# Kernel optimization log

Measured on AMD Instinct MI355X. Metric: run time of the kernel, lower is better.

Reference implementation:

```python
import jax, jax.numpy as jnp
import numpy as np

# module hyperparams (match init_kwargs)
C, K, S, RATIO, GC = 64, 7, 2, 2, 16
G = C // GC                      # 4 groups
KK = K * K                       # 49
NS = int(RATIO * S)              # 4
NN = NS * NS                     # 16
PAD = (K - 1) // 2               # 3
C1_IN = G * (2 * K * GC + KK)    # 1092
C1_OUT = G * NN * KK // 10       # 313
C2_OUT = G * NN * KK             # 3136
EPS = 1e-5


def _unfold(x, k, s, p):
    # torch.nn.Unfold: patches ordered (C, ki, kj) channel-major
    B, Cc, H, W = x.shape
    xp = jnp.pad(x, ((0, 0), (0, 0), (p, p), (p, p)))
    Ho = (H + 2 * p - k) // s + 1
    Wo = (W + 2 * p - k) // s + 1
    rows = jnp.arange(Ho)[:, None] * s + jnp.arange(k)[None, :]      # (Ho,k)
    cols = jnp.arange(Wo)[:, None] * s + jnp.arange(k)[None, :]      # (Wo,k)
    pat = xp[:, :, rows[:, :, None, None], cols[None, None, :, :]]   # (B,C,Ho,k,Wo,k)
    return pat.transpose(0, 1, 3, 5, 2, 4)                            # (B,C,k,k,Ho,Wo)


def setup_inputs() -> dict:
    key = jax.random.key(0)
    ks = jax.random.split(key, 5)
    x = jax.random.normal(ks[0], (8, C, 64, 64), dtype=jnp.float32)
    w1 = jax.random.normal(ks[1], (C1_OUT, C1_IN), dtype=jnp.float32) * 0.02
    gamma = jnp.ones((C1_OUT,), dtype=jnp.float32)   # BN weight (constant_init 1)
    beta = jnp.zeros((C1_OUT,), dtype=jnp.float32)   # BN bias
    w2 = jax.random.normal(ks[2], (C2_OUT, C1_OUT), dtype=jnp.float32) * 0.02
    b2 = jnp.zeros((C2_OUT,), dtype=jnp.float32)
    return {"x": x, "w1": w1, "gamma": gamma, "beta": beta, "w2": w2, "b2": b2}


def reference(x, w1, gamma, beta, w2, b2):
    B, _, H, W = x.shape
    pat = _unfold(x, K, S, PAD)                          # (B,C,K,K,Ho,Wo)
    Ho, Wo = pat.shape[-2], pat.shape[-1]
    xg = pat.reshape(B, G, GC, K, K, Ho, Wo)
    # three axis-wise max pools -> per-pixel descriptor
    x1 = xg.max(axis=2).reshape(B, G * K * K, Ho, Wo)
    x2 = xg.max(axis=3).reshape(B, G * GC * K, Ho, Wo)
    x3 = xg.max(axis=4).reshape(B, G * GC * K, Ho, Wo)
    feat = jnp.concatenate([x1, x2, x3], axis=1)         # (B, C1_IN, Ho, Wo)
    # conv1: 1x1 conv (no bias) + BN (batch stats) + ReLU
    h = jnp.einsum('bchw,oc->bohw', feat, w1)
    mu = h.mean(axis=(0, 2, 3), keepdims=True)
    var = h.var(axis=(0, 2, 3), keepdims=True)
    h = gamma[None, :, None, None] * (h - mu) * jax.lax.rsqrt(var + EPS) + beta[None, :, None, None]
    h = jax.nn.relu(h)
    # conv2: 1x1 conv with bias
    h2 = jnp.einsum('bchw,oc->bohw', h, w2) + b2[None, :, None, None]
    wt = h2.reshape(B, G, KK, NN, Ho, Wo)
    wt = jax.nn.softmax(wt, axis=2)                      # softmax over kernel positions
    # softmax-weighted patch reduction (mean over k*k)
    xk = xg.reshape(B, G, GC, KK, Ho, Wo)
    out = jnp.einsum('bgckhw,bgknhw->bgcnhw', xk, wt) / KK
    out = out.reshape(B, C, NS, NS, Ho, Wo)
    out = out.transpose(0, 1, 4, 2, 5, 3).reshape(B, C, Ho * NS, Wo * NS)
    return out
```

## Files before the change

### kernel.cpp

```cpp
#include <hip/hip_runtime.h>

namespace {
constexpr int kB    = 8;
constexpr int kC    = 64;
constexpr int kH    = 64, kW = 64;
constexpr int kNP   = 8192;
constexpr int kC1In = 1092;
constexpr int kKP   = 1152;
constexpr int kC1Out= 313;
constexpr int kC2Out= 3136;
constexpr int kC1P  = 320;
constexpr int kRowS = 56;
constexpr int kPosS = 16 * kRowS + 8;
constexpr int kPreFeat = 2048;
constexpr int kPreW2   = 490;
constexpr int kPreW1   = 1440;
constexpr int kPreBlocks = kPreFeat + kPreW2 + kPreW1;
}

typedef __attribute__((ext_vector_type(8))) short bf16x8;
typedef __attribute__((ext_vector_type(8))) _Float16 f16x8;
typedef __attribute__((ext_vector_type(2))) _Float16 h16x2;
typedef __attribute__((ext_vector_type(4))) float f32x4;

__device__ __forceinline__ unsigned short f2bf(float f) {
    unsigned u = __float_as_uint(f);
    unsigned r = (u + 0x7fffu + ((u >> 16) & 1u)) >> 16;
    return (unsigned short)r;
}
__device__ __forceinline__ float bf2f(unsigned short h) {
    return __uint_as_float(((unsigned)h) << 16);
}

__global__ __launch_bounds__(256) void k_pre(const float* __restrict__ x,
        const float* __restrict__ w1, const float* __restrict__ w2,
        unsigned short* __restrict__ feat_bf, unsigned short* __restrict__ w1s,
        bf16x8* __restrict__ w2t, float* __restrict__ stats) {
    __shared__ float xs[16 * 7 * 40];
    int tid = threadIdx.x;
    int bid = blockIdx.x;

    if (bid < kPreFeat) {
        int g = bid >> 9, pt = bid & 511;
        int p0 = pt * 16;
        int b = p0 >> 10, i = (p0 >> 5) & 31, j0 = p0 & 31;
        int y0 = 2 * i - 3, xbase = 2 * j0 - 3;
        const float* xb = x + ((size_t)(b * 64 + g * 16) << 12);

        for (int idx = tid; idx < 16 * 7 * 40; idx += 256) {
            int ch = idx / 280, r2 = idx - ch * 280;
            int row = r2 / 40, col = r2 - row * 40;
            int yy = y0 + row, xx = xbase + col;
            float v = 0.f;
            if ((unsigned)yy < 64u && (unsigned)xx < 64u)
                v = xb[(ch << 12) + (yy << 6) + xx];
            xs[idx] = v;
        }
        __syncthreads();

        for (int pos = 0; pos < 16; ++pos) {
            for (int c = tid; c < 273; c += 256) {
                float m = -INFINITY;
                int cg;
                if (c < 49) {
                    int a = c / 7, bk = c - a * 7;
                    int base = a * 40 + 2 * pos + bk;
                    #pragma unroll
                    for (int ch = 0; ch < 16; ++ch) m = fmaxf(m, xs[ch * 280 + base]);
                    cg = g * 49 + c;
                } else if (c < 161) {
                    int r = c - 49;
                    int ch = r / 7, bk = r - ch * 7;
                    int base = ch * 280 + 2 * pos + bk;
                    #pragma unroll
                    for (int a = 0; a < 7; ++a) m = fmaxf(m, xs[base + a * 40]);
                    cg = 196 + g * 112 + r;
                } else {
                    int r = c - 161;
                    int ch = r / 7, a = r - ch * 7;
                    int base = ch * 280 + a * 40 + 2 * pos;
                    #pragma unroll
                    for (int bk = 0; bk < 7; ++bk) m = fmaxf(m, xs[base + bk]);
                    cg = 644 + g * 112 + r;
                }
                feat_bf[(size_t)(p0 + pos) * kKP + cg] = f2bf(m);
            }
        }
        if (g == 3) {
            for (int idx = tid; idx < 16 * 60; idx += 256) {
                int pos = idx / 60, c = idx - pos * 60;
                feat_bf[(size_t)(p0 + pos) * kKP + 1092 + c] = 0;
            }
        }
    } else if (bid < kPreFeat + kPreW2) {
        int idx = (bid - kPreFeat) * 256 + tid;
        int lane = idx & 63;
        int t = (idx >> 6) % 10;
        int k = (idx / 640) % 49;
        int g = idx / 31360;
        int n = lane & 15, c0 = t * 32 + ((lane >> 4) << 3);
        int row = g * 784 + k * 16 + n;
        bf16x8 hi;
        #pragma unroll
        for (int e = 0; e < 8; ++e) {
            int c = c0 + e;
            float v = (c < kC1Out) ? w2[(size_t)row * kC1Out + c] : 0.f;
            hi[e] = (short)f2bf(v);
        }
        w2t[idx] = hi;
    } else {
        int idx = (bid - kPreFeat - kPreW2) * 256 + tid;
        if (idx < 640) stats[idx] = 0.f;
        int r = idx / kKP, c = idx - r * kKP;
        float v = (r < kC1Out && c < kC1In) ? w1[(size_t)r * kC1In + c] : 0.f;
        w1s[idx] = f2bf(v);
    }
}

__global__ __launch_bounds__(512) void k_gemm1(
        const unsigned short* __restrict__ feat_bf, const unsigned short* __restrict__ w1s,
        unsigned short* __restrict__ hb16, float* __restrict__ sum_, float* __restrict__ sumsq_) {
    __shared__ unsigned short Ald[128 * 64];
    __shared__ unsigned short Bld[64 * 64];
    __shared__ float lsum[64], lsq[64];
    int tid = threadIdx.x;
    int lane = tid & 63, wv = tid >> 6;
    int row0 = blockIdx.x * 128, col0 = blockIdx.y * 64;
    int wr = wv >> 1, wc = wv & 1;
    int srow = lane >> 3;
    int soct = (lane & 7) ^ srow;
    int frow = lane & 15, fk = lane >> 4;

    f32x4 acc[2][2] = {};
    for (int k0 = 0; k0 < kKP; k0 += 64) {
        #pragma unroll
        for (int qq = 0; qq < 3; ++qq) {
            int q = wv + qq * 8;
            const unsigned short* srcbase;
            unsigned short* dst;
            int grow;
            if (q < 16) { grow = row0 + q * 8 + srow; srcbase = feat_bf; dst = Ald + q * 512; }
            else        { grow = col0 + (q - 16) * 8 + srow; srcbase = w1s; dst = Bld + (q - 16) * 512; }
            const unsigned short* src = srcbase + (size_t)grow * kKP + k0 + soct * 8;
            __builtin_amdgcn_global_load_lds(
                (const __attribute__((address_space(1))) unsigned int*)src,
                (__attribute__((address_space(3))) unsigned int*)dst, 16, 0, 0);
        }
        __syncthreads();
        #pragma unroll
        for (int ks = 0; ks < 2; ++ks) {
            int oct = ks * 4 + fk;
            bf16x8 a0, a1, b0, b1;
            { int r = wr * 32 + frow;      a0 = *(const bf16x8*)(Ald + (r * 8 + (oct ^ (r & 7))) * 8); }
            { int r = wr * 32 + 16 + frow; a1 = *(const bf16x8*)(Ald + (r * 8 + (oct ^ (r & 7))) * 8); }
            { int r = wc * 32 + frow;      b0 = *(const bf16x8*)(Bld + (r * 8 + (oct ^ (r & 7))) * 8); }
            { int r = wc * 32 + 16 + frow; b1 = *(const bf16x8*)(Bld + (r * 8 + (oct ^ (r & 7))) * 8); }
            acc[0][0] = __builtin_amdgcn_mfma_f32_16x16x32_bf16(a0, b0, acc[0][0], 0, 0, 0);
            acc[0][1] = __builtin_amdgcn_mfma_f32_16x16x32_bf16(a0, b1, acc[0][1], 0, 0, 0);
            acc[1][0] = __builtin_amdgcn_mfma_f32_16x16x32_bf16(a1, b0, acc[1][0], 0, 0, 0);
            acc[1][1] = __builtin_amdgcn_mfma_f32_16x16x32_bf16(a1, b1, acc[1][1], 0, 0, 0);
        }
        __syncthreads();
    }

    if (tid < 64) { lsum[tid] = 0.f; lsq[tid] = 0.f; }
    __syncthreads();
    #pragma unroll
    for (int j = 0; j < 2; ++j) {
        int col_l = wc * 32 + j * 16 + (lane & 15);
        float s = 0.f, sq = 0.f;
        #pragma unroll
        for (int i = 0; i < 2; ++i) {
            int mrow = row0 + wr * 32 + i * 16 + (lane >> 4) * 4;
            #pragma unroll
            for (int r = 0; r < 4; ++r) {
                float v = acc[i][j][r];
                hb16[(size_t)(mrow + r) * kC1P + col0 + col_l] = f2bf(v);
                s += v; sq += v * v;
            }
        }
        s  += __shfl_xor(s, 16);  s  += __shfl_xor(s, 32);
        sq += __shfl_xor(sq, 16); sq += __shfl_xor(sq, 32);
        if (lane < 16) {
            atomicAdd(&lsum[col_l], s);
            atomicAdd(&lsq[col_l], sq);
        }
    }
    __syncthreads();
    if (tid < 64 && col0 + tid < kC1Out) {
        atomicAdd(&sum_[col0 + tid], lsum[tid]);
        atomicAdd(&sumsq_[col0 + tid], lsq[tid]);
    }
}

__global__ void k_split_h(const unsigned short* __restrict__ hb16,
                          const float* __restrict__ sum_, const float* __restrict__ sumsq_,
                          const float* __restrict__ gamma, const float* __restrict__ beta,
                          bf16x8* __restrict__ ht_hi) {
    int idx = blockIdx.x * 256 + threadIdx.x;
    int lane = idx & 63;
    int t = (idx >> 6) % 10;
    int ptile = idx / 640;
    int pos = ptile * 16 + (lane & 15);
    int c0 = t * 32 + ((lane >> 4) << 3);
    bf16x8 raw = *(const bf16x8*)(hb16 + (size_t)pos * kC1P + c0);
    bf16x8 hi;
    #pragma unroll
    for (int e = 0; e < 8; ++e) {
        int c = c0 + e;
        float v = 0.f;
        if (c < kC1Out) {
            float mu  = sum_[c]   * (1.f / kNP);
            float var = sumsq_[c] * (1.f / kNP) - mu * mu;
            float sc  = gamma[c] * rsqrtf(var + 1e-5f);
            float sh  = beta[c] - mu * sc;
            v = fmaxf(bf2f((unsigned short)raw[e]) * sc + sh, 0.f);
        }
        hi[e] = (short)f2bf(v);
    }
    ht_hi[idx] = hi;
}

__global__ __launch_bounds__(512) void k_fused(
        const bf16x8* __restrict__ ht_hi, const bf16x8* __restrict__ w2t,
        const float* __restrict__ b2, const float* __restrict__ x,
        float* __restrict__ out) {
    __shared__ _Float16 wtb[32 * kPosS];
    __shared__ float invt[512];
    __shared__ bf16x8 htl[1280];
    int tid = threadIdx.x;
    int lane = tid & 63, wv = tid >> 6;
    int bid = blockIdx.x;
    int g = bid >> 8, pt = bid & 255;

    {
        const bf16x8* hb = ht_hi + (size_t)(pt * 2) * 640;
        #pragma unroll
        for (int r = 0; r < 3; ++r) {
            int idx = r * 512 + tid;
            if (idx < 1280)
                __builtin_amdgcn_global_load_lds(
                    (const __attribute__((address_space(1))) unsigned int*)(hb + idx),
                    (__attribute__((address_space(3))) unsigned int*)(htl + idx), 16, 0, 0);
        }
    }
    __syncthreads();

    int col = lane & 15, rgrp = lane >> 4;
    for (int k = wv; k < 49; k += 16) {
        int k2 = k + 8;
        bool has2 = (k2 < 49);
        int k2c = has2 ? k2 : k;
        f32x4 acc00 = {0.f,0.f,0.f,0.f}, acc01 = {0.f,0.f,0.f,0.f};
        f32x4 acc10 = {0.f,0.f,0.f,0.f}, acc11 = {0.f,0.f,0.f,0.f};
        const bf16x8* wb0 = w2t + ((size_t)(g * 49 + k)   * 10) * 64 + lane;
        const bf16x8* wb1 = w2t + ((size_t)(g * 49 + k2c) * 10) * 64 + lane;
        bf16x8 bh0[10], bh1[10];
        #pragma unroll
        for (int t = 0; t < 10; ++t) { bh0[t] = wb0[t * 64]; bh1[t] = wb1[t * 64]; }
        #pragma unroll
        for (int t = 0; t < 10; ++t) {
            bf16x8 a0 = htl[t * 64 + lane];
            bf16x8 a1 = htl[640 + t * 64 + lane];
            acc00 = __builtin_amdgcn_mfma_f32_16x16x32_bf16(a0, bh0[t], acc00, 0, 0, 0);
            acc01 = __builtin_amdgcn_mfma_f32_16x16x32_bf16(a1, bh0[t], acc01, 0, 0, 0);
            acc10 = __builtin_amdgcn_mfma_f32_16x16x32_bf16(a0, bh1[t], acc10, 0, 0, 0);
            acc11 = __builtin_amdgcn_mfma_f32_16x16x32_bf16(a1, bh1[t], acc11, 0, 0, 0);
        }
        {
            float bias = b2[g * 784 + k * 16 + col];
            #pragma unroll
            for (int r = 0; r < 4; ++r) {
                int pos = rgrp * 4 + r;
                wtb[pos * kPosS + k * 16 + col]        = (_Float16)(acc00[r] + bias);
                wtb[(pos + 16) * kPosS + k * 16 + col] = (_Float16)(acc01[r] + bias);
            }
        }
        if (has2) {
            float bias = b2[g * 784 + k2 * 16 + col];
            #pragma unroll
            for (int r = 0; r < 4; ++r) {
                int pos = rgrp * 4 + r;
                wtb[pos * kPosS + k2 * 16 + col]        = (_Float16)(acc10[r] + bias);
                wtb[(pos + 16) * kPosS + k2 * 16 + col] = (_Float16)(acc11[r] + bias);
            }
        }
    }
    __syncthreads();

    {
        int pos = tid >> 4, n = tid & 15;
        const _Float16* baseA = wtb + pos * kPosS + n;
        f16x8 ee[7];
        float m = -INFINITY;
        #pragma unroll
        for (int c = 0; c < 7; ++c)
            #pragma unroll
            for (int e = 0; e < 8; ++e) {
                int k = c * 8 + e;
                if (k < 49) {
                    _Float16 v = baseA[k * 16];
                    ee[c][e] = v;
                    m = fmaxf(m, (float)v);
                } else ee[c][e] = (_Float16)0.f;
            }
        float s = 0.f;
        #pragma unroll
        for (int c = 0; c < 7; ++c)
            #pragma unroll
            for (int e = 0; e < 8; ++e) {
                int k = c * 8 + e;
                if (k < 49) {
                    float ex = __expf((float)ee[c][e] - m);
                    s += ex;
                    ee[c][e] = (_Float16)ex;
                }
            }
        __syncthreads();
        _Float16* baseB = wtb + pos * kPosS + n * kRowS;
        #pragma unroll
        for (int c = 0; c < 7; ++c) *(f16x8*)(baseB + c * 8) = ee[c];
        invt[tid] = 1.f / (s * 49.f);
    }
    __syncthreads();

    {
        int pos = tid & 31, c16 = tid >> 5;
        int p = pt * 32 + pos;
        int b = p >> 10, i = (p >> 5) & 31, j = p & 31;
        int y0 = 2 * i - 3, x0c = 2 * j - 3;
        const float* xc = x + (((size_t)b * 64 + g * 16 + c16) << 12);
        h16x2 patch2[28];
        #pragma unroll
        for (int a = 0; a < 7; ++a) {
            int yy = y0 + a;
            #pragma unroll
            for (int bk = 0; bk < 7; ++bk) {
                int kk = a * 7 + bk, xx = x0c + bk;
                float v = ((unsigned)yy < 64u && (unsigned)xx < 64u)
                        ? xc[(yy << 6) + xx] : 0.f;
                patch2[kk >> 1][kk & 1] = (_Float16)v;
            }
        }
        patch2[24][1] = (_Float16)0.f;
        patch2[25] = (h16x2)(_Float16)0.f;
        patch2[26] = (h16x2)(_Float16)0.f;
        patch2[27] = (h16x2)(_Float16)0.f;

        const _Float16* prow = wtb + pos * kPosS;
        float* outb = out + (((size_t)b * 64 + g * 16 + c16) << 14);
        #pragma unroll
        for (int n1 = 0; n1 < 4; ++n1) {
            f32x4 st;
            #pragma unroll
            for (int n2 = 0; n2 < 4; ++n2) {
                int n = n1 * 4 + n2;
                const f16x8* row = (const f16x8*)(prow + n * kRowS);
                float acc = 0.f;
                #pragma unroll
                for (int c = 0; c < 7; ++c) {
                    f16x8 w = row[c];
                    #pragma unroll
                    for (int q = 0; q < 4; ++q) {
                        h16x2 wp; wp[0] = w[2 * q]; wp[1] = w[2 * q + 1];
                        acc = __builtin_amdgcn_fdot2(patch2[c * 4 + q], wp, acc, false);
                    }
                }
                st[n2] = acc * invt[pos * 16 + n];
            }
            *(f32x4*)(outb + (i * 4 + n1) * 128 + j * 4) = st;
        }
    }
}

extern "C" void kernel_launch(void* const* d_in, const int* in_sizes, int n_in,
                              void* d_out, int out_size, void* d_ws, size_t ws_size,
                              hipStream_t stream) {
    const float* x     = (const float*)d_in[0];
    const float* w1    = (const float*)d_in[1];
    const float* gamma = (const float*)d_in[2];
    const float* beta  = (const float*)d_in[3];
    const float* w2    = (const float*)d_in[4];
    const float* b2    = (const float*)d_in[5];
    float* out = (float*)d_out;

    float* ws = (float*)d_ws;
    unsigned short* feat_bf = (unsigned short*)ws;
    unsigned short* hb16 = (unsigned short*)(ws + 4718592);
    float* w2t_f   = ws + 4718592 + 1310720;
    unsigned short* w1s = (unsigned short*)(w2t_f + 501760);
    float* sum_   = w2t_f + 501760 + 184320;
    float* sumsq_ = sum_ + 320;

    bf16x8* ht_hi = (bf16x8*)ws;
    bf16x8* w2t   = (bf16x8*)w2t_f;

    k_pre<<<kPreBlocks, 256, 0, stream>>>(x, w1, w2, feat_bf, w1s, w2t, sum_);
    k_gemm1<<<dim3(kNP / 128, 5), 512, 0, stream>>>(feat_bf, w1s, hb16, sum_, sumsq_);
    k_split_h<<<1280, 256, 0, stream>>>(hb16, sum_, sumsq_, gamma, beta, ht_hi);
    k_fused<<<1024, 512, 0, stream>>>(ht_hi, w2t, b2, x, out);
}
```

Baseline: 109.4 us.

## Compute softmax-weighted patch reduction with bf16 MFMA using LDS-staged input tile

The final reduction over the 49 kernel positions changes from per-thread fdot2 loops to two 16x16x32 bf16 MFMA instructions per position. The A operand is 16 channels by K positions and the B operand is K positions by 16 outputs. The block's 16-channel, 7-row input strip is staged once into LDS as bf16, reusing the ht buffer, so each thread no longer issues 49 scattered global loads for its own patch. Softmax weights are now stored as bf16 instead of fp16, which lowers precision. Output stores become scalar, strided by channel, instead of float4 vectors.

```diff
diff --git a/kernel.cpp b/kernel.cpp
--- a/kernel.cpp
+++ b/kernel.cpp
@@ -16,11 +16,12 @@
 constexpr int kPreW2   = 490;
 constexpr int kPreW1   = 1440;
 constexpr int kPreBlocks = kPreFeat + kPreW2 + kPreW1;
+constexpr int kXlsC = 70;
+constexpr int kXlsCh = 7 * kXlsC;
 }
 
 typedef __attribute__((ext_vector_type(8))) short bf16x8;
 typedef __attribute__((ext_vector_type(8))) _Float16 f16x8;
-typedef __attribute__((ext_vector_type(2))) _Float16 h16x2;
 typedef __attribute__((ext_vector_type(4))) float f32x4;
 
 __device__ __forceinline__ unsigned short f2bf(float f) {
@@ -232,6 +233,8 @@
     int lane = tid & 63, wv = tid >> 6;
     int bid = blockIdx.x;
     int g = bid >> 8, pt = bid & 255;
+    int bb = pt >> 5, ii = pt & 31;
+    int y0 = 2 * ii - 3;
 
     {
         const bf16x8* hb = ht_hi + (size_t)(pt * 2) * 640;
@@ -288,87 +291,90 @@
     }
     __syncthreads();
 
+    unsigned short* xls = (unsigned short*)htl;
+    {
+        const float* xg = x + (((size_t)bb * 64 + g * 16) << 12);
+        for (int idx = tid; idx < 16 * kXlsCh; idx += 512) {
+            int ch = idx / kXlsCh, r2 = idx - ch * kXlsCh;
+            int a = r2 / kXlsC, cc = r2 - a * kXlsC;
+            int yy = y0 + a, xx = cc - 3;
+            float v = 0.f;
+            if ((unsigned)yy < 64u && (unsigned)xx < 64u)
+                v = xg[(ch << 12) + (yy << 6) + xx];
+            xls[idx] = f2bf(v);
+        }
+    }
+
     {
         int pos = tid >> 4, n = tid & 15;
         const _Float16* baseA = wtb + pos * kPosS + n;
-        f16x8 ee[7];
+        float vv[49];
         float m = -INFINITY;
         #pragma unroll
-        for (int c = 0; c < 7; ++c)
+        for (int k = 0; k < 49; ++k) {
+            float v = (float)baseA[k * 16];
+            vv[k] = v;
+            m = fmaxf(m, v);
+        }
+        float s = 0.f;
+        #pragma unroll
+        for (int k = 0; k < 49; ++k) {
+            float ex = __expf(vv[k] - m);
+            s += ex;
+            vv[k] = ex;
+        }
+        __syncthreads();
+        unsigned short* baseB = (unsigned short*)(wtb + pos * kPosS + n * kRowS);
+        #pragma unroll
+        for (int c = 0; c < 7; ++c) {
+            bf16x8 sb;
             #pragma unroll
             for (int e = 0; e < 8; ++e) {
                 int k = c * 8 + e;
-                if (k < 49) {
-                    _Float16 v = baseA[k * 16];
-                    ee[c][e] = v;
-                    m = fmaxf(m, (float)v);
-                } else ee[c][e] = (_Float16)0.f;
-            }
-        float s = 0.f;
-        #pragma unroll
-        for (int c = 0; c < 7; ++c)
+                sb[e] = (k < 49) ? (short)f2bf(vv[k]) : (short)0;
+            }
+            *(bf16x8*)(baseB + c * 8) = sb;
+        }
+        invt[tid] = 1.f / (s * 49.f);
+    }
+    __syncthreads();
+
+    {
+        int nidx = lane & 15, oct = lane >> 4;
+        float* outg = out + (((size_t)bb * 64 + g * 16) << 14);
+        #pragma unroll
+        for (int pp = 0; pp < 4; ++pp) {
+            int pos = wv * 4 + pp;
+            const unsigned short* xrow = xls + nidx * kXlsCh;
+            bf16x8 a0, a1;
             #pragma unroll
             for (int e = 0; e < 8; ++e) {
-                int k = c * 8 + e;
-                if (k < 49) {
-                    float ex = __expf((float)ee[c][e] - m);
-                    s += ex;
-                    ee[c][e] = (_Float16)ex;
+                int k = oct * 8 + e;
+                int a = k / 7, bk = k - a * 7;
+                a0[e] = (short)xrow[a * kXlsC + 2 * pos + bk];
+                int kk = 32 + oct * 8 + e;
+                short v = 0;
+                if (kk < 49) {
+                    int a2 = kk / 7, bk2 = kk - a2 * 7;
+                    v = (short)xrow[a2 * kXlsC + 2 * pos + bk2];
                 }
-            }
-        __syncthreads();
-        _Float16* baseB = wtb + pos * kPosS + n * kRowS;
-        #pragma unroll
-        for (int c = 0; c < 7; ++c) *(f16x8*)(baseB + c * 8) = ee[c];
-        invt[tid] = 1.f / (s * 49.f);
-    }
-    __syncthreads();
-
-    {
-        int pos = tid & 31, c16 = tid >> 5;
-        int p = pt * 32 + pos;
-        int b = p >> 10, i = (p >> 5) & 31, j = p & 31;
-        int y0 = 2 * i - 3, x0c = 2 * j - 3;
-        const float* xc = x + (((size_t)b * 64 + g * 16 + c16) << 12);
-        h16x2 patch2[28];
-        #pragma unroll
-        for (int a = 0; a < 7; ++a) {
-            int yy = y0 + a;
-            #pragma unroll
-            for (int bk = 0; bk < 7; ++bk) {
-                int kk = a * 7 + bk, xx = x0c + bk;
-                float v = ((unsigned)yy < 64u && (unsigned)xx < 64u)
-                        ? xc[(yy << 6) + xx] : 0.f;
-                patch2[kk >> 1][kk & 1] = (_Float16)v;
-            }
-        }
-        patch2[24][1] = (_Float16)0.f;
-        patch2[25] = (h16x2)(_Float16)0.f;
-        patch2[26] = (h16x2)(_Float16)0.f;
-        patch2[27] = (h16x2)(_Float16)0.f;
-
-        const _Float16* prow = wtb + pos * kPosS;
-        float* outb = out + (((size_t)b * 64 + g * 16 + c16) << 14);
-        #pragma unroll
-        for (int n1 = 0; n1 < 4; ++n1) {
-            f32x4 st;
-            #pragma unroll
-            for (int n2 = 0; n2 < 4; ++n2) {
-                int n = n1 * 4 + n2;
-                const f16x8* row = (const f16x8*)(prow + n * kRowS);
-                float acc = 0.f;
-                #pragma unroll
-                for (int c = 0; c < 7; ++c) {
-                    f16x8 w = row[c];
-                    #pragma unroll
-                    for (int q = 0; q < 4; ++q) {
-                        h16x2 wp; wp[0] = w[2 * q]; wp[1] = w[2 * q + 1];
-                        acc = __builtin_amdgcn_fdot2(patch2[c * 4 + q], wp, acc, false);
-                    }
-                }
-                st[n2] = acc * invt[pos * 16 + n];
-            }
-            *(f32x4*)(outb + (i * 4 + n1) * 128 + j * 4) = st;
+                a1[e] = v;
+            }
+            const unsigned short* erow = (const unsigned short*)(wtb + pos * kPosS + nidx * kRowS);
+            bf16x8 b0 = *(const bf16x8*)(erow + oct * 8);
+            bf16x8 b1 = *(const bf16x8*)(erow + 32 + oct * 8);
+            if (oct == 3) b1 = (bf16x8){0,0,0,0,0,0,0,0};
+            f32x4 acc = {0.f, 0.f, 0.f, 0.f};
+            acc = __builtin_amdgcn_mfma_f32_16x16x32_bf16(a0, b0, acc, 0, 0, 0);
+            acc = __builtin_amdgcn_mfma_f32_16x16x32_bf16(a1, b1, acc, 0, 0, 0);
+            float scv = invt[pos * 16 + nidx];
+            int n1 = nidx >> 2, n2 = nidx & 3;
+            float* outp = outg + (ii * 4 + n1) * 128 + pos * 4 + n2;
+            #pragma unroll
+            for (int r = 0; r < 4; ++r) {
+                int c16 = oct * 4 + r;
+                outp[(size_t)c16 << 14] = acc[r] * scv;
+            }
         }
     }
 }
```

New measurement: 117.7 us. 1.08x slower.
